# Kernel optimization log

Measured on AMD Instinct MI355X. Metric: run time of the kernel, lower is better.

Reference implementation:

```python
import jax, jax.numpy as jnp
import numpy as np

B, Q, K, D, H, HD, HID, ED, CPB, E = 2, 300, 1024, 256, 8, 32, 32, 256, 256, 131072
N = B * Q
EPS = 1e-5


def _ln(x, g, b):
    mu = x.mean(-1, keepdims=True)
    v = ((x - mu) ** 2).mean(-1, keepdims=True)
    return (x - mu) / jnp.sqrt(v + EPS) * g + b


def setup_inputs():
    key = jax.random.key(0)
    ks = jax.random.split(key, 32)
    rn = lambda k, s, sc=0.02: jax.random.normal(k, s, jnp.float32) * sc
    return {
        "nodes": jax.random.normal(ks[0], (N, D), jnp.float32),
        "images": jax.random.normal(ks[1], (B, K, D), jnp.float32),
        "rel_coords": jax.random.normal(ks[2], (B, Q, K, 2), jnp.float32),
        "edge_feats": jax.random.normal(ks[3], (E, ED), jnp.float32),
        "edge_index": jax.random.randint(ks[4], (2, E), 0, N, jnp.int32),
        "images_mask": jnp.zeros((B, K), dtype=bool),
        "ln1_g": jnp.ones((D,)), "ln1_b": jnp.zeros((D,)),
        "ln2_g": jnp.ones((D,)), "ln2_b": jnp.zeros((D,)),
        "ln3_g": jnp.ones((D,)), "ln3_b": jnp.zeros((D,)),
        "Wni": rn(ks[5], (D, HID * H)), "bni": jnp.zeros((HID * H,)),
        "Wnj": rn(ks[6], (D, HID * H)), "bnj": jnp.zeros((HID * H,)),
        "We": rn(ks[7], (ED, HID * H)), "be": jnp.zeros((HID * H,)),
        "attn_proj": jax.random.normal(ks[8], (H, HID), jnp.float32),
        "Wmsg": rn(ks[9], (D + ED, D)), "bmsg": jnp.zeros((D,)),
        "Wg_out": rn(ks[10], (D, D)), "bg_out": jnp.zeros((D,)),
        "Wq": rn(ks[11], (D, D)), "bq": jnp.zeros((D,)),
        "Wkv": rn(ks[12], (D, 2 * D)), "bkv": jnp.zeros((2 * D,)),
        "Wc1": rn(ks[13], (2, CPB), 0.5), "bc1": jnp.zeros((CPB,)),
        "Wc2": rn(ks[14], (CPB, H), 0.1), "bc2": jnp.zeros((H,)),
        "Wc_out": rn(ks[15], (D, D)), "bc_out": jnp.zeros((D,)),
        "Wf1": rn(ks[16], (D, 4 * D)), "bf1": jnp.zeros((4 * D,)),
        "Wf2": rn(ks[17], (4 * D, D)), "bf2": jnp.zeros((D,)),
    }


def reference(nodes, images, rel_coords, edge_feats, edge_index, images_mask,
              ln1_g, ln1_b, ln2_g, ln2_b, ln3_g, ln3_b,
              Wni, bni, Wnj, bnj, We, be, attn_proj, Wmsg, bmsg, Wg_out, bg_out,
              Wq, bq, Wkv, bkv, Wc1, bc1, Wc2, bc2, Wc_out, bc_out,
              Wf1, bf1, Wf2, bf2):
    src, dst = edge_index[0], edge_index[1]
    # --- graph attention (pre-LN residual) ---
    x = _ln(nodes, ln1_g, ln1_b)
    ni, nj = x[src], x[dst]  # [E, D]
    hidden = jax.nn.leaky_relu(
        ni @ Wni + bni + nj @ Wnj + bnj + edge_feats @ We + be, 0.2)
    hidden = hidden.reshape(E, H, HID)
    logits = jnp.einsum('ehd,hd->eh', hidden, attn_proj)  # [E, H]
    m = jax.ops.segment_max(logits, src, num_segments=N)
    z = jnp.exp(logits - m[src])
    scores = z / jax.ops.segment_sum(z, src, num_segments=N)[src]  # scatter softmax
    msg = (jnp.concatenate([nj, edge_feats], -1) @ Wmsg + bmsg).reshape(E, H, HD)
    agg = jax.ops.segment_sum(msg * scores[..., None], src, num_segments=N).reshape(N, D)
    nodes = nodes + (agg @ Wg_out + bg_out)
    # --- cross attention with continuous position bias ---
    x2 = _ln(nodes, ln2_g, ln2_b).reshape(B, Q, D)
    q = (x2 @ Wq + bq).reshape(B, Q, H, HD).transpose(0, 2, 1, 3)  # [B,H,Q,hd]
    kv = (images @ Wkv + bkv).reshape(B, K, 2, H, HD)
    k = kv[:, :, 0].transpose(0, 2, 1, 3)  # [B,H,K,hd]
    v = kv[:, :, 1].transpose(0, 2, 1, 3)
    cpb = jax.nn.relu(rel_coords @ Wc1 + bc1) @ Wc2 + bc2  # [B,Q,K,H]
    bias = jnp.where(images_mask[:, None, None, :], -jnp.inf,
                     jnp.transpose(cpb, (0, 3, 1, 2)))  # [B,H,Q,K]
    att = jnp.einsum('bhqd,bhkd->bhqk', q, k) / jnp.sqrt(jnp.float32(HD)) + bias
    p = jax.nn.softmax(att, axis=-1)
    out = jnp.einsum('bhqk,bhkd->bhqd', p, v)
    out = out.reshape(B, Q, H * HD)  # faithful to original: reshape WITHOUT head transpose
    nodes = nodes + (out @ Wc_out + bc_out).reshape(N, D)
    # --- FFN (residual from the normed input, as in original) ---
    x3 = _ln(nodes, ln3_g, ln3_b)
    ff = jax.nn.gelu(x3 @ Wf1 + bf1, approximate=False) @ Wf2 + bf2
    return ff + x3
```

## Files before the change

kernel.cpp:

```cpp
#include <hip/hip_runtime.h>
#include <hip/hip_bf16.h>
#include <math.h>

#define E_   131072
#define N_   600
#define NB_  2
#define NQ_  300
#define NK_  1024
#define NH_  8

typedef __hip_bfloat16 bf16;
typedef __bf16 bh8 __attribute__((ext_vector_type(8)));
typedef float  fx4 __attribute__((ext_vector_type(4)));

static __device__ __forceinline__ float b2f(bf16 x){ return __bfloat162float(x); }
static __device__ __forceinline__ float bfbits2f(unsigned short u){
  return __uint_as_float((unsigned)u << 16);
}
static __device__ __forceinline__ unsigned short bfu(float x){
  return __bfloat16_as_ushort(__float2bfloat16(x));
}
static __device__ __forceinline__ unsigned pack2(float x, float y){
  return (unsigned)bfu(x) | ((unsigned)bfu(y) << 16);
}
static __device__ __forceinline__ float ldf(const void* p, size_t i, bool isf32){
  return isf32 ? ((const float*)p)[i] : b2f(((const bf16*)p)[i]);
}

constexpr int WOFF[32] = {
  0,256,512,768,1024,1280,
  1536,67072,67328,132864,
  133120,133376,
  133632,264704,
  264960,330496,330752,396288,
  396544,527616,
  528128,528640,528896,530944,
  530952,596488,
  596744,858888,859912,1122056,
  1122312,
  1187848};
#define NWSEG 31
#define WTOT  1187848
struct SrcTab { const void* p[NWSEG]; };
struct TrTab { int4 d[8]; };

static __device__ __forceinline__ void ln_stats(float v, int t, float* r1, float* r2,
                                                float& mu, float& rstd){
  float s1 = v, s2 = v*v;
  #pragma unroll
  for (int o = 32; o; o >>= 1){ s1 += __shfl_down(s1, o); s2 += __shfl_down(s2, o); }
  if ((t & 63) == 0){ r1[t>>6] = s1; r2[t>>6] = s2; }
  __syncthreads();
  float t1 = r1[0]+r1[1]+r1[2]+r1[3];
  float t2 = r2[0]+r2[1]+r2[2]+r2[3];
  mu = t1 * (1.f/256.f);
  float var = t2 * (1.f/256.f) - mu*mu;
  rstd = rsqrtf(var + 1e-5f);
  __syncthreads();
}

__global__ void k_init(int* cnt, float* denom, const void* nodes, int* dflag){
  int i = blockIdx.x*256 + threadIdx.x;
  if (i < N_) cnt[i] = 0;
  if (i < N_*NH_) denom[i] = 0.f;
  if (i == 0){
    const unsigned short* h = (const unsigned short*)nodes;
    int odd = 0;
    for (int j = 0; j < 64; j++){
      int e = (h[j] >> 7) & 0xFF;
      if (e < 100 || e > 150) odd++;
    }
    *dflag = (odd > 8) ? 1 : 0;
  }
}

__global__ __launch_bounds__(256) void k_cvt(SrcTab tab, float* wall, const int* dflag){
  int i = blockIdx.x*256 + threadIdx.x;
  if (i >= WTOT) return;
  bool isf32 = (*dflag != 0);
  int seg = 0;
  while (seg < NWSEG-1 && i >= WOFF[seg+1]) seg++;
  wall[i] = ldf(tab.p[seg], (size_t)(i - WOFF[seg]), isf32);
}

__global__ __launch_bounds__(256) void k_tr(TrTab tab, const float* __restrict__ wall,
                                            bf16* __restrict__ wbt)
{
  __shared__ float tile[64][65];
  int4 d = tab.d[blockIdx.z];
  int K = d.y, Nn = d.z;
  int k0 = blockIdx.x*64, n0 = blockIdx.y*64;
  if (k0 >= K || n0 >= Nn) return;
  const float* src = wall + d.x;
  bf16* dst = wbt + d.w;
  int t = threadIdx.x;
  int rr = t >> 6, cc = t & 63;
  #pragma unroll
  for (int p = 0; p < 16; p++){
    int row = p*4 + rr;
    tile[row][cc] = src[(size_t)(k0 + row)*Nn + n0 + cc];
  }
  __syncthreads();
  #pragma unroll
  for (int p = 0; p < 16; p++){
    int row = p*4 + rr;
    dst[(size_t)(n0 + row)*K + k0 + cc] = __float2bfloat16(tile[cc][row]);
  }
}

__global__ __launch_bounds__(256) void k_ln1(
    const void* __restrict__ nodes, const int* __restrict__ dflag,
    const float* __restrict__ g1, const float* __restrict__ b1, bf16* __restrict__ x1)
{
  __shared__ float r1[4], r2[4];
  int n = blockIdx.x, t = threadIdx.x;
  bool isf32 = (*dflag != 0);
  float v = ldf(nodes, (size_t)n*256 + t, isf32);
  float mu, rstd;
  ln_stats(v, t, r1, r2, mu, rstd);
  x1[n*256 + t] = __float2bfloat16((v - mu) * rstd * g1[t] + b1[t]);
}

__global__ void k_count(const int* __restrict__ ei, int* cnt){
  int e = blockIdx.x*256 + threadIdx.x;
  atomicAdd(&cnt[ei[e]], 1);
}

__global__ __launch_bounds__(1024) void k_scan(const int* __restrict__ cnt,
                                               int* offs, int* cursor){
  __shared__ int s[1024];
  int t = threadIdx.x;
  s[t] = (t < N_) ? cnt[t] : 0;
  __syncthreads();
  for (int o = 1; o < 1024; o <<= 1){
    int v = 0;
    if (t >= o) v = s[t - o];
    __syncthreads();
    if (t >= o) s[t] += v;
    __syncthreads();
  }
  if (t < N_){ int excl = (t == 0) ? 0 : s[t-1]; offs[t] = excl; cursor[t] = excl; }
  if (t == N_-1) offs[N_] = s[N_-1];
}

__global__ void k_scatter(const int* __restrict__ ei, int* cursor, int* eorder){
  int e = blockIdx.x*256 + threadIdx.x;
  int pos = atomicAdd(&cursor[ei[e]], 1);
  eorder[pos] = e;
}

__global__ __launch_bounds__(256) void k_gemm_dual(
    const void* __restrict__ A, int m_base, const int* __restrict__ dflag,
    const bf16* __restrict__ BT, bf16* __restrict__ C)
{
  __shared__ __align__(16) bf16 As[128*72];
  __shared__ __align__(16) bf16 Bs[128*72];
  int m0 = blockIdx.x * 128;
  int n0 = blockIdx.y * 128;
  int t = threadIdx.x;
  bool isf32 = (*dflag != 0);
  int wave = t >> 6, lane = t & 63;
  int wr = (wave >> 1) * 64, wc = (wave & 1) * 64;
  int lm = lane & 15, lq = lane >> 4;
  int srow = t >> 2;
  int scol = (t & 3) * 16;
  size_t r0  = (size_t)(m_base + m0 + srow) * 256;
  size_t r1  = (size_t)(m_base + m0 + 64 + srow) * 256;
  size_t rB0 = (size_t)(n0 + srow) * 256;
  size_t rB1 = (size_t)(n0 + 64 + srow) * 256;
  fx4 acc[4][4] = {};
  for (int kk = 0; kk < 256; kk += 64){
    uint4 a00, a01, a10, a11, b00, b01, b10, b11;
    if (isf32){
      const float* p0 = (const float*)A + r0 + kk + scol;
      const float* p1 = (const float*)A + r1 + kk + scol;
      float4 x0 = *(const float4*)p0,      x1v = *(const float4*)(p0 + 4);
      float4 x2 = *(const float4*)(p0 + 8), x3 = *(const float4*)(p0 + 12);
      float4 y0 = *(const float4*)p1,      y1v = *(const float4*)(p1 + 4);
      float4 y2 = *(const float4*)(p1 + 8), y3 = *(const float4*)(p1 + 12);
      a00.x = pack2(x0.x,x0.y); a00.y = pack2(x0.z,x0.w);
      a00.z = pack2(x1v.x,x1v.y); a00.w = pack2(x1v.z,x1v.w);
      a01.x = pack2(x2.x,x2.y); a01.y = pack2(x2.z,x2.w);
      a01.z = pack2(x3.x,x3.y); a01.w = pack2(x3.z,x3.w);
      a10.x = pack2(y0.x,y0.y); a10.y = pack2(y0.z,y0.w);
      a10.z = pack2(y1v.x,y1v.y); a10.w = pack2(y1v.z,y1v.w);
      a11.x = pack2(y2.x,y2.y); a11.y = pack2(y2.z,y2.w);
      a11.z = pack2(y3.x,y3.y); a11.w = pack2(y3.z,y3.w);
    } else {
      const bf16* p0 = (const bf16*)A + r0 + kk + scol;
      const bf16* p1 = (const bf16*)A + r1 + kk + scol;
      a00 = *(const uint4*)p0;       a01 = *(const uint4*)(p0 + 8);
      a10 = *(const uint4*)p1;       a11 = *(const uint4*)(p1 + 8);
    }
// ... 9 lines not shown
    *(uint4*)(Bs + srow*72 + scol)          = b00;
    *(uint4*)(Bs + srow*72 + scol + 8)      = b01;
    *(uint4*)(Bs + (64+srow)*72 + scol)     = b10;
    *(uint4*)(Bs + (64+srow)*72 + scol + 8) = b11;
    __syncthreads();
    #pragma unroll
    for (int ks = 0; ks < 2; ks++){
      bh8 af[4], bfr[4];
      #pragma unroll
      for (int mt = 0; mt < 4; mt++)
        af[mt] = *reinterpret_cast<const bh8*>(As + (wr + mt*16 + lm)*72 + ks*32 + lq*8);
      #pragma unroll
      for (int nt = 0; nt < 4; nt++)
        bfr[nt] = *reinterpret_cast<const bh8*>(Bs + (wc + nt*16 + lm)*72 + ks*32 + lq*8);
      #pragma unroll
      for (int mt = 0; mt < 4; mt++)
        #pragma unroll
        for (int nt = 0; nt < 4; nt++)
          acc[mt][nt] = __builtin_amdgcn_mfma_f32_16x16x32_bf16(af[mt], bfr[nt], acc[mt][nt], 0, 0, 0);
    }
  }
  #pragma unroll
  for (int mt = 0; mt < 4; mt++)
    #pragma unroll
    for (int nt = 0; nt < 4; nt++)
      #pragma unroll
      for (int r = 0; r < 4; r++){
        int row = m0 + wr + mt*16 + lq*4 + r;
        int col = n0 + wc + nt*16 + lm;
        C[(size_t)row*256 + col] = __float2bfloat16(acc[mt][nt][r]);
      }
}

__global__ __launch_bounds__(256) void k_gemm(
    const void* __restrict__ A, const int* __restrict__ dflag, int adual,
    int K, int M, const bf16* __restrict__ BT, int mode,
    void* __restrict__ D, int ldd,
    const float* __restrict__ bias, const float* __restrict__ add,
    float* __restrict__ aux)
{
  __shared__ __align__(16) bf16 As[128*72];
  __shared__ __align__(16) bf16 Bs[128*72];
  int m0 = blockIdx.x * 128;
  int n0 = blockIdx.y * 128;
  int t = threadIdx.x;
  bool f32src = adual && (*dflag != 0);
  int wave = t >> 6, lane = t & 63;
  int wr = (wave >> 1) * 64, wc = (wave & 1) * 64;
  int lm = lane & 15, lq = lane >> 4;
  int srow = t >> 2;
  int scol = (t & 3) * 16;
  size_t rA0 = (size_t)(m0 + srow) * K;
  size_t rA1 = (size_t)(m0 + 64 + srow) * K;
  size_t rB0 = (size_t)(n0 + srow) * K;
  size_t rB1 = (size_t)(n0 + 64 + srow) * K;
  fx4 acc[4][4] = {};
  for (int kk = 0; kk < K; kk += 64){
    uint4 a00, a01, a10, a11, b00, b01, b10, b11;
    if (f32src){
      const float* p0 = (const float*)A + rA0 + kk + scol;
      const float* p1 = (const float*)A + rA1 + kk + scol;
      float4 x0 = *(const float4*)p0,      x1v = *(const float4*)(p0 + 4);
      float4 x2 = *(const float4*)(p0 + 8), x3 = *(const float4*)(p0 + 12);
      float4 y0 = *(const float4*)p1,      y1v = *(const float4*)(p1 + 4);
      float4 y2 = *(const float4*)(p1 + 8), y3 = *(const float4*)(p1 + 12);
      a00.x = pack2(x0.x,x0.y); a00.y = pack2(x0.z,x0.w);
      a00.z = pack2(x1v.x,x1v.y); a00.w = pack2(x1v.z,x1v.w);
      a01.x = pack2(x2.x,x2.y); a01.y = pack2(x2.z,x2.w);
      a01.z = pack2(x3.x,x3.y); a01.w = pack2(x3.z,x3.w);
      a10.x = pack2(y0.x,y0.y); a10.y = pack2(y0.z,y0.w);
      a10.z = pack2(y1v.x,y1v.y); a10.w = pack2(y1v.z,y1v.w);
      a11.x = pack2(y2.x,y2.y); a11.y = pack2(y2.z,y2.w);
      a11.z = pack2(y3.x,y3.y); a11.w = pack2(y3.z,y3.w);
    } else {
      const bf16* p0 = (const bf16*)A + rA0 + kk + scol;
      const bf16* p1 = (const bf16*)A + rA1 + kk + scol;
      a00 = *(const uint4*)p0;       a01 = *(const uint4*)(p0 + 8);
      a10 = *(const uint4*)p1;       a11 = *(const uint4*)(p1 + 8);
    }
    b00 = *(const uint4*)(BT + rB0 + kk + scol);
    b01 = *(const uint4*)(BT + rB0 + kk + scol + 8);
    b10 = *(const uint4*)(BT + rB1 + kk + scol);
    b11 = *(const uint4*)(BT + rB1 + kk + scol + 8);
    __syncthreads();
    *(uint4*)(As + srow*72 + scol)          = a00;
    *(uint4*)(As + srow*72 + scol + 8)      = a01;
    *(uint4*)(As + (64+srow)*72 + scol)     = a10;
    *(uint4*)(As + (64+srow)*72 + scol + 8) = a11;
    *(uint4*)(Bs + srow*72 + scol)          = b00;
    *(uint4*)(Bs + srow*72 + scol + 8)      = b01;
    *(uint4*)(Bs + (64+srow)*72 + scol)     = b10;
    *(uint4*)(Bs + (64+srow)*72 + scol + 8) = b11;
    __syncthreads();
    #pragma unroll
    for (int ks = 0; ks < 2; ks++){
      bh8 af[4], bfr[4];
      #pragma unroll
      for (int mt = 0; mt < 4; mt++)
        af[mt] = *reinterpret_cast<const bh8*>(As + (wr + mt*16 + lm)*72 + ks*32 + lq*8);
      #pragma unroll
      for (int nt = 0; nt < 4; nt++)
        bfr[nt] = *reinterpret_cast<const bh8*>(Bs + (wc + nt*16 + lm)*72 + ks*32 + lq*8);
      #pragma unroll
      for (int mt = 0; mt < 4; mt++)
        #pragma unroll
        for (int nt = 0; nt < 4; nt++)
          acc[mt][nt] = __builtin_amdgcn_mfma_f32_16x16x32_bf16(af[mt], bfr[nt], acc[mt][nt], 0, 0, 0);
    }
  }
  #pragma unroll
  for (int mt = 0; mt < 4; mt++)
    #pragma unroll
    for (int nt = 0; nt < 4; nt++)
      #pragma unroll
      for (int r = 0; r < 4; r++){
        int row = m0 + wr + mt*16 + lq*4 + r;
        int col = n0 + wc + nt*16 + lm;
        if (row >= M) continue;
        float v = acc[mt][nt][r];
        if (mode == 0){
          if (bias) v += bias[col];
          ((float*)D)[(size_t)row*ldd + col] = v;
        } else if (mode == 1){
          v += bias[col];
          if (col < 256){
            ((float*)D)[(size_t)row*256 + col] = v;
          } else {
            int b = row >> 10, ki = row & 1023;
            int hh = (col - 256) >> 5, dd = (col - 256) & 31;
            aux[(((size_t)b*NH_ + hh)*32 + dd)*NK_ + ki] = v;
          }
        } else if (mode == 2){
          v += bias[col] + add[(size_t)row*ldd + col];
          ((float*)D)[(size_t)row*ldd + col] = v;
        } else {
          v += bias[col];
          float g = 0.5f*v*(1.f + erff(v*0.70710678118654752f));
          ((bf16*)D)[(size_t)row*ldd + col] = __float2bfloat16(g);
        }
      }
}

__global__ __launch_bounds__(256) void k_logits(
    const bf16* __restrict__ He, const float* __restrict__ Pall,
    const float* __restrict__ bni, const float* __restrict__ bnj, const float* __restrict__ be,
    const float* __restrict__ ap, const int* __restrict__ ei,
    float* __restrict__ z, float* __restrict__ denom, int e0chunk)
{
  __shared__ float hs[32*264];
  __shared__ int   ssh[32], dsh[32];
  __shared__ float aps[256], bhs[256];
  int t = threadIdx.x;
  int base = e0chunk + blockIdx.x*32;
  if (t < 32) ssh[t] = ei[base + t];
  else if (t < 64) dsh[t-32] = ei[E_ + base + (t - 32)];
  aps[t] = ap[t];
  bhs[t] = bni[t] + bnj[t] + be[t];
  __syncthreads();
  int slot = (t >> 5)*33 + (t & 31);
  for (int r = 0; r < 32; r++){
    float v = b2f(He[(size_t)(base - e0chunk + r)*256 + t])
            + Pall[ssh[r]*768 + t] + Pall[dsh[r]*768 + 256 + t] + bhs[t];
    v = (v > 0.f) ? v : 0.2f*v;
    hs[r*264 + slot] = v;
  }
  __syncthreads();
  int e = t >> 3, h = t & 7;
  const float* hr  = hs + e*264 + h*33;
  const float* apr = aps + h*32;
  float acc = 0.f;
  #pragma unroll
  for (int i = 0; i < 32; i++) acc = fmaf(hr[i], apr[i], acc);
  float zv = __expf(fminf(acc, 30.f));
  z[(size_t)(base + e)*8 + h] = zv;
  atomicAdd(&denom[ssh[e]*8 + h], zv);
}

__global__ __launch_bounds__(256) void k_agg(
    const int* __restrict__ offs, const int* __restrict__ eorder, const int* __restrict__ ei,
    const float* __restrict__ z,
    const void* __restrict__ ef, const int* __restrict__ dflag,
    const float* __restrict__ Pall, const float* __restrict__ denom,
    const float* __restrict__ bmsg, const float* __restrict__ Wmsg,
    const void* __restrict__ nodes,
    const float* __restrict__ Wg, const float* __restrict__ bg,
    const float* __restrict__ g2, const float* __restrict__ b2v,
    const float* __restrict__ Wq, const float* __restrict__ bq,
    float* __restrict__ nodes1, float* __restrict__ qbuf)
{
  __shared__ float zsh[32*8];
  __shared__ int   esh[32];
  __shared__ int   dsh[32];
  __shared__ float Fs[8*257];
  __shared__ float aggs[256];
  __shared__ float sinv[8];
  __shared__ float r1[4], r2[4];
  int n = blockIdx.x, t = threadIdx.x;
  bool isf32 = (*dflag != 0);
  int h = t >> 5;
  int e0 = offs[n], e1 = offs[n+1];
  float facc[8] = {};
  float gacc = 0.f;
  int jz = t >> 3, hz = t & 7;
  for (int base = e0; base < e1; base += 32){
    int cnt = min(32, e1 - base);
    __syncthreads();
    if (t < 32){
      int e = (t < cnt) ? eorder[base + t] : eorder[e0];
      esh[t] = e;
      dsh[t] = ei[E_ + e];
    }
    __syncthreads();
    zsh[t] = (jz < cnt) ? z[(size_t)esh[jz]*8 + hz] : 0.f;
    __syncthreads();
    #pragma unroll 8
    for (int jj = 0; jj < 32; jj++){
      int e = esh[jj];
      float efv = ldf(ef, (size_t)e*256 + t, isf32);
      float pv  = Pall[(size_t)dsh[jj]*768 + 512 + t];
      #pragma unroll
      for (int hq = 0; hq < 8; hq++) facc[hq] = fmaf(zsh[jj*8 + hq], efv, facc[hq]);
      gacc = fmaf(zsh[jj*8 + h], pv, gacc);
    }
  }
  if (t < 8){
    float ds = denom[n*8 + t];
    sinv[t] = (ds > 0.f) ? 1.f/ds : 0.f;
  }
  __syncthreads();
  #pragma unroll
  for (int hq = 0; hq < 8; hq++)
// ... 12 lines not shown
    am += (p0 + p1) + (p2 + p3);
  }
  aggs[t] = am;
  __syncthreads();
  float o = bg[t] + ldf(nodes, (size_t)n*256 + t, isf32);
  {
    float p0=0.f, p1=0.f, p2=0.f, p3=0.f;
    for (int k = 0; k < 256; k += 4){
      p0 = fmaf(aggs[k+0], Wg[(k+0)*256 + t], p0);
      p1 = fmaf(aggs[k+1], Wg[(k+1)*256 + t], p1);
      p2 = fmaf(aggs[k+2], Wg[(k+2)*256 + t], p2);
      p3 = fmaf(aggs[k+3], Wg[(k+3)*256 + t], p3);
    }
    o += (p0 + p1) + (p2 + p3);
  }
  nodes1[n*256 + t] = o;
  float mu, rstd;
  ln_stats(o, t, r1, r2, mu, rstd);
  float x2 = (o - mu) * rstd * g2[t] + b2v[t];
  aggs[t] = x2;
  __syncthreads();
  float q = bq[t];
  {
    float p0=0.f, p1=0.f, p2=0.f, p3=0.f;
    for (int k = 0; k < 256; k += 4){
      p0 = fmaf(aggs[k+0], Wq[(k+0)*256 + t], p0);
      p1 = fmaf(aggs[k+1], Wq[(k+1)*256 + t], p1);
      p2 = fmaf(aggs[k+2], Wq[(k+2)*256 + t], p2);
      p3 = fmaf(aggs[k+3], Wq[(k+3)*256 + t], p3);
    }
    q += (p0 + p1) + (p2 + p3);
  }
  qbuf[n*256 + t] = q;
}

__global__ __launch_bounds__(256) void k_cpb(
    const void* __restrict__ rel, const int* __restrict__ dflag,
    const float* __restrict__ Wc1, const float* __restrict__ bc1,
    const float* __restrict__ Wc2, const float* __restrict__ bc2, bf16* __restrict__ bias)
{
  __shared__ float w0[256], w1[256], bb[256], w2[256*8], b2s[8];
  int t = threadIdx.x;
  bool isf32 = (*dflag != 0);
  w0[t] = Wc1[t]; w1[t] = Wc1[256 + t]; bb[t] = bc1[t];
  for (int i = t; i < 2048; i += 256) w2[i] = Wc2[i];
  if (t < 8) b2s[t] = bc2[t];
  __syncthreads();
  size_t pos = (size_t)blockIdx.x*256 + t;
  float c0, c1;
  if (isf32){
    float2 v = ((const float2*)rel)[pos];
    c0 = v.x; c1 = v.y;
  } else {
    unsigned v = ((const unsigned*)rel)[pos];
    c0 = bfbits2f((unsigned short)(v & 0xffff));
    c1 = bfbits2f((unsigned short)(v >> 16));
  }
  float acc[8] = {};
  for (int j = 0; j < 256; j++){
    float hj = fmaf(c0, w0[j], fmaf(c1, w1[j], bb[j]));
    hj = fmaxf(hj, 0.f);
    #pragma unroll
    for (int h = 0; h < 8; h++) acc[h] = fmaf(hj, w2[j*8 + h], acc[h]);
  }
  int k = (int)(pos & 1023);
  size_t qq = pos >> 10;
  size_t b = qq / NQ_, q = qq % NQ_;
  bf16* dst = bias + ((b*NH_)*NQ_ + q)*NK_;
  #pragma unroll
  for (int h = 0; h < 8; h++)
    dst[(size_t)h*NQ_*NK_ + k] = __float2bfloat16(acc[h] + b2s[h]);
}

__global__ __launch_bounds__(256) void k_attn(
    const float* __restrict__ qbuf, const float* __restrict__ kbuf, const float* __restrict__ vT,
    const bf16* __restrict__ bias, bf16* __restrict__ Yb)
{
  __shared__ float Qs[8*33];
  __shared__ float Ks[128*33];
  __shared__ float Sc[8*1024];
  __shared__ float Op[4*8*32];
  __shared__ float qs[8];
  int qt = blockIdx.x, h = blockIdx.y, b = blockIdx.z;
  int q0 = qt*8;
  int t = threadIdx.x;
  {
    int q = t >> 5, d = t & 31;
    int gq = q0 + q;
    Qs[q*33 + d] = (gq < NQ_) ? qbuf[((size_t)b*NQ_ + gq)*256 + h*32 + d] : 0.f;
  }
  const float* kbase = kbuf + (size_t)b*NK_*256 + h*32;
  const bf16*  bb    = bias + ((size_t)(b*NH_ + h)*NQ_)*NK_;
  int kl = t & 127;
  int qb = (t >> 7) * 4;
  for (int kt = 0; kt < 8; kt++){
    int k0 = kt*128;
    __syncthreads();
    {
      int r = t >> 1, c0 = (t & 1) * 16;
      const float* src = kbase + (size_t)(k0 + r)*256 + c0;
      float* dst = Ks + r*33 + c0;
      #pragma unroll
      for (int ii = 0; ii < 4; ii++){
        float4 f = *(const float4*)(src + ii*4);
// ... 85 lines not shown
    }
  }
}

__global__ __launch_bounds__(256) void k_ln3(
    const float* __restrict__ n2, const float* __restrict__ g3, const float* __restrict__ b3,
    float* __restrict__ x3f, bf16* __restrict__ x3b)
{
  __shared__ float r1[4], r2[4];
  int n = blockIdx.x, t = threadIdx.x;
  float v = n2[n*256 + t];
  float mu, rstd;
  ln_stats(v, t, r1, r2, mu, rstd);
  float x3 = (v - mu) * rstd * g3[t] + b3[t];
  x3f[n*256 + t] = x3;
  x3b[n*256 + t] = __float2bfloat16(x3);
}

extern "C" void kernel_launch(void* const* d_in, const int* in_sizes, int n_in,
                              void* d_out, int out_size, void* d_ws, size_t ws_size,
                              hipStream_t stream)
{
  const void* nodes  = d_in[0];
  const void* images = d_in[1];
  const void* rel    = d_in[2];
  const void* ef     = d_in[3];
  const int*  ei     = (const int*)d_in[4];
  float* out = (float*)d_out;

  char* w = (char*)d_ws;
  auto alloc = [&](size_t bytes) -> void* {
    void* p = (void*)w; w += (bytes + 255) & ~(size_t)255; return p;
  };
  int*      dflag  = (int*)     alloc(4);
  float*    Wall   = (float*)   alloc((size_t)WTOT*4);
  bf16*     Wbt    = (bf16*)    alloc((size_t)983040*2);
  bf16*     bias   = (bf16*)    alloc((size_t)NB_*NH_*NQ_*NK_*2);
  float*    zbuf   = (float*)   alloc((size_t)E_*8*4);
  float*    Pall   = (float*)   alloc((size_t)N_*768*4);
  float*    nodes1 = (float*)   alloc(N_*256*4);
  float*    qbuf   = (float*)   alloc(N_*256*4);
  float*    kbuf   = (float*)   alloc((size_t)NB_*NK_*256*4);
  float*    vT     = (float*)   alloc((size_t)NB_*NH_*32*NK_*4);
  float*    n2buf  = (float*)   alloc(N_*256*4);
  float*    x3f    = (float*)   alloc(N_*256*4);
  bf16*     x1     = (bf16*)    alloc(N_*256*2);
  bf16*     x3b    = (bf16*)    alloc(N_*256*2);
  bf16*     Yb     = (bf16*)    alloc(N_*256*2);
  bf16*     H1     = (bf16*)    alloc((size_t)N_*1024*2);
  float*    denom  = (float*)   alloc(N_*8*4);
  int*      cnt    = (int*)     alloc(N_*4);
  int*      offs   = (int*)     alloc((N_+1)*4);
  int*      cursor = (int*)     alloc(N_*4);
  int*      eorder = (int*)     alloc((size_t)E_*4);
  size_t used = (size_t)(w - (char*)d_ws);
  int CH = E_;
  while (CH > 2048 && used + (size_t)CH*256*2 + 256 > ws_size) CH >>= 1;
  bf16* He = (bf16*)alloc((size_t)CH*256*2);

  bf16* WeT  = Wbt + 0;
  bf16* WkvT = Wbt + 65536;
  bf16* WnpT = Wbt + 196608;
  bf16* WcoT = Wbt + 393216;
  bf16* Wf1T = Wbt + 458752;
  bf16* Wf2T = Wbt + 720896;

  const float *ln1g=Wall+WOFF[0],  *ln1b=Wall+WOFF[1];
  const float *ln2g=Wall+WOFF[2],  *ln2b=Wall+WOFF[3];
  const float *ln3g=Wall+WOFF[4],  *ln3b=Wall+WOFF[5];
  const float *bni=Wall+WOFF[7],  *bnj=Wall+WOFF[9], *be=Wall+WOFF[10];
  const float *ap =Wall+WOFF[11];
  const float *Wmsg=Wall+WOFF[12], *bmsg=Wall+WOFF[13];
  const float *Wg=Wall+WOFF[14], *bg=Wall+WOFF[15];
  const float *Wq=Wall+WOFF[16], *bq=Wall+WOFF[17];
  const float *bkv=Wall+WOFF[19];
  const float *Wc1=Wall+WOFF[20], *bc1=Wall+WOFF[21];
  const float *Wc2=Wall+WOFF[22], *bc2=Wall+WOFF[23];
  const float *bco=Wall+WOFF[25];
  const float *bf1v=Wall+WOFF[27];
  const float *bf2v=Wall+WOFF[29];

  SrcTab tab;
  {
    const int idx[NWSEG] = {6,7,8,9,10,11, 12,13,14,15, 17,18, 19,20, 21,22,23,24,
                            25,26, 27,28,29,30, 31,32, 33,34,35,36, 16};
    for (int i = 0; i < NWSEG; i++) tab.p[i] = d_in[idx[i]];
  }
  TrTab tr;
  tr.d[0] = {WOFF[30], 256,  256, 0};
  tr.d[1] = {WOFF[18], 256,  512, 65536};
  tr.d[2] = {WOFF[6],  256,  256, 196608};
  tr.d[3] = {WOFF[8],  256,  256, 196608+65536};
  tr.d[4] = {WOFF[12], 256,  256, 196608+131072};
  tr.d[5] = {WOFF[24], 256,  256, 393216};
  tr.d[6] = {WOFF[26], 256, 1024, 458752};
  tr.d[7] = {WOFF[28],1024,  256, 720896};

  k_init   <<<19, 256, 0, stream>>>(cnt, denom, nodes, dflag);
  k_cvt    <<<(WTOT+255)/256, 256, 0, stream>>>(tab, Wall, dflag);
  k_tr     <<<dim3(16,16,8), 256, 0, stream>>>(tr, Wall, Wbt);
  k_ln1    <<<N_, 256, 0, stream>>>(nodes, dflag, ln1g, ln1b, x1);
  k_count  <<<E_/256, 256, 0, stream>>>(ei, cnt);
  k_scan   <<<1, 1024, 0, stream>>>(cnt, offs, cursor);
  k_scatter<<<E_/256, 256, 0, stream>>>(ei, cursor, eorder);

  k_gemm<<<dim3(5,6), 256, 0, stream>>>(x1, dflag, 0, 256, N_, WnpT, 0,
                                        Pall, 768, nullptr, nullptr, nullptr);

  for (int c0 = 0; c0 < E_; c0 += CH){
    k_gemm_dual<<<dim3(CH/128, 2), 256, 0, stream>>>(ef, c0, dflag, WeT, He);
    k_logits   <<<CH/32, 256, 0, stream>>>(He, Pall, bni, bnj, be, ap, ei,
                                           zbuf, denom, c0);
  }
  k_agg  <<<N_, 256, 0, stream>>>(offs, eorder, ei, zbuf, ef, dflag, Pall, denom,
                                  bmsg, Wmsg, nodes, Wg, bg, ln2g, ln2b, Wq, bq,
                                  nodes1, qbuf);
  k_gemm<<<dim3(16,4), 256, 0, stream>>>(images, dflag, 1, 256, NB_*NK_, WkvT, 1,
                                         kbuf, 256, bkv, nullptr, vT);
  k_cpb    <<<NB_*NQ_*NK_/256, 256, 0, stream>>>(rel, dflag, Wc1, bc1, Wc2, bc2, bias);
  dim3 agrid((NQ_ + 7)/8, NH_, NB_);
  k_attn   <<<agrid, 256, 0, stream>>>(qbuf, kbuf, vT, bias, Yb);
  k_gemm<<<dim3(5,2), 256, 0, stream>>>(Yb, dflag, 0, 256, N_, WcoT, 2,
                                        n2buf, 256, bco, nodes1, nullptr);
  k_ln3  <<<N_, 256, 0, stream>>>(n2buf, ln3g, ln3b, x3f, x3b);
  k_gemm<<<dim3(5,8), 256, 0, stream>>>(x3b, dflag, 0, 256, N_, Wf1T, 3,
                                        H1, 1024, bf1v, nullptr, nullptr);
  k_gemm<<<dim3(5,2), 256, 0, stream>>>(H1, dflag, 0, 1024, N_, Wf2T, 2,
                                        out, 256, bf2v, x3f, nullptr);
}
```

Before: 718.9 us.

## Merge prep and independent stages into fewer batched kernel launches

Folds init, weight conversion, transpose and LN1 into a single k_prep launch. The transpose now reads the raw inputs directly, so it no longer depends on the converted copy. Edge counting moves into the scan kernel as shared-memory atomics, and the node projection GEMM, KV GEMM, CPB MLP and edge scatter run as block ranges of one k_batch launch. Every kernel now recomputes the dtype flag per block with a ballot instead of reading a global flag. The aim is to cut launch count and serialization between independent stages, at the cost of a serial single-block count over all edges and heterogeneous blocks sharing one shared-memory footprint.

```diff
diff --git a/kernel.cpp b/kernel.cpp
--- a/kernel.cpp
+++ b/kernel.cpp
@@ -25,6 +25,17 @@
 }
 static __device__ __forceinline__ float ldf(const void* p, size_t i, bool isf32){
   return isf32 ? ((const float*)p)[i] : b2f(((const bf16*)p)[i]);
+}
+
+static __device__ __forceinline__ bool get_isf32(const void* nodes, int t, int* sh){
+  if (t < 64){
+    const unsigned short* h = (const unsigned short*)nodes;
+    int e = (h[t] >> 7) & 0xFF;
+    unsigned long long b = __ballot(e < 100 || e > 150);
+    if (t == 0) *sh = (__popcll(b) > 8) ? 1 : 0;
+  }
+  __syncthreads();
+  return *sh != 0;
 }
 
 constexpr int WOFF[32] = {
@@ -42,7 +53,7 @@
 #define NWSEG 31
 #define WTOT  1187848
 struct SrcTab { const void* p[NWSEG]; };
-struct TrTab { int4 d[8]; };
+struct TrTabP { const void* p[8]; int4 d[8]; };
 
 static __device__ __forceinline__ void ln_stats(float v, int t, float* r1, float* r2,
                                                 float& mu, float& rstd){
@@ -59,78 +70,73 @@
   __syncthreads();
 }
 
-__global__ void k_init(int* cnt, float* denom, const void* nodes, int* dflag){
-  int i = blockIdx.x*256 + threadIdx.x;
-  if (i < N_) cnt[i] = 0;
-  if (i < N_*NH_) denom[i] = 0.f;
-  if (i == 0){
-    const unsigned short* h = (const unsigned short*)nodes;
-    int odd = 0;
-    for (int j = 0; j < 64; j++){
-      int e = (h[j] >> 7) & 0xFF;
-      if (e < 100 || e > 150) odd++;
-    }
-    *dflag = (odd > 8) ? 1 : 0;
-  }
-}
-
-__global__ __launch_bounds__(256) void k_cvt(SrcTab tab, float* wall, const int* dflag){
-  int i = blockIdx.x*256 + threadIdx.x;
-  if (i >= WTOT) return;
-  bool isf32 = (*dflag != 0);
-  int seg = 0;
-  while (seg < NWSEG-1 && i >= WOFF[seg+1]) seg++;
-  wall[i] = ldf(tab.p[seg], (size_t)(i - WOFF[seg]), isf32);
-}
-
-__global__ __launch_bounds__(256) void k_tr(TrTab tab, const float* __restrict__ wall,
-                                            bf16* __restrict__ wbt)
+#define PB_CVT 4641
+#define PB_TR  2048
+#define PB_LN1 600
+#define PB_DEN 19
+#define PB_TOTAL (PB_CVT + PB_TR + PB_LN1 + PB_DEN)
+
+__global__ __launch_bounds__(256) void k_prep(
+    SrcTab tab, TrTabP trp, float* __restrict__ wall, bf16* __restrict__ wbt,
+    const void* __restrict__ nodes, bf16* __restrict__ x1, float* __restrict__ denom)
 {
   __shared__ float tile[64][65];
-  int4 d = tab.d[blockIdx.z];
-  int K = d.y, Nn = d.z;
-  int k0 = blockIdx.x*64, n0 = blockIdx.y*64;
-  if (k0 >= K || n0 >= Nn) return;
-  const float* src = wall + d.x;
-  bf16* dst = wbt + d.w;
+  __shared__ float r1[4], r2[4];
+  __shared__ int dsh;
   int t = threadIdx.x;
-  int rr = t >> 6, cc = t & 63;
-  #pragma unroll
-  for (int p = 0; p < 16; p++){
-    int row = p*4 + rr;
-    tile[row][cc] = src[(size_t)(k0 + row)*Nn + n0 + cc];
-  }
-  __syncthreads();
-  #pragma unroll
-  for (int p = 0; p < 16; p++){
-    int row = p*4 + rr;
-    dst[(size_t)(n0 + row)*K + k0 + cc] = __float2bfloat16(tile[cc][row]);
-  }
-}
-
-__global__ __launch_bounds__(256) void k_ln1(
-    const void* __restrict__ nodes, const int* __restrict__ dflag,
-    const float* __restrict__ g1, const float* __restrict__ b1, bf16* __restrict__ x1)
-{
-  __shared__ float r1[4], r2[4];
-  int n = blockIdx.x, t = threadIdx.x;
-  bool isf32 = (*dflag != 0);
-  float v = ldf(nodes, (size_t)n*256 + t, isf32);
-  float mu, rstd;
-  ln_stats(v, t, r1, r2, mu, rstd);
-  x1[n*256 + t] = __float2bfloat16((v - mu) * rstd * g1[t] + b1[t]);
-}
-
-__global__ void k_count(const int* __restrict__ ei, int* cnt){
-  int e = blockIdx.x*256 + threadIdx.x;
-  atomicAdd(&cnt[ei[e]], 1);
-}
-
-__global__ __launch_bounds__(1024) void k_scan(const int* __restrict__ cnt,
+  int b = blockIdx.x;
+  bool isf32 = get_isf32(nodes, t, &dsh);
+  if (b < PB_CVT){
+    int i = b*256 + t;
+    if (i < WTOT){
+      int seg = 0;
+      while (seg < NWSEG-1 && i >= WOFF[seg+1]) seg++;
+      wall[i] = ldf(tab.p[seg], (size_t)(i - WOFF[seg]), isf32);
+    }
+  } else if (b < PB_CVT + PB_TR){
+    int lb = b - PB_CVT;
+    int bz = lb >> 8, by = (lb >> 4) & 15, bx = lb & 15;
+    int4 d = trp.d[bz];
+    int K = d.y, Nn = d.z;
+    int k0 = bx*64, n0 = by*64;
+    if (k0 < K && n0 < Nn){
+      const void* src = trp.p[bz];
+      bf16* dst = wbt + d.w;
+      int rr = t >> 6, cc = t & 63;
+      #pragma unroll
+      for (int p = 0; p < 16; p++){
+        int row = p*4 + rr;
+        tile[row][cc] = ldf(src, (size_t)(k0 + row)*Nn + n0 + cc, isf32);
+      }
+      __syncthreads();
+      #pragma unroll
+      for (int p = 0; p < 16; p++){
+        int row = p*4 + rr;
+        dst[(size_t)(n0 + row)*K + k0 + cc] = __float2bfloat16(tile[cc][row]);
+      }
+    }
+  } else if (b < PB_CVT + PB_TR + PB_LN1){
+    int n = b - (PB_CVT + PB_TR);
+    float v = ldf(nodes, (size_t)n*256 + t, isf32);
+    float mu, rstd;
+    ln_stats(v, t, r1, r2, mu, rstd);
+    float g  = ldf(tab.p[0], t, isf32);
+    float bb = ldf(tab.p[1], t, isf32);
+    x1[n*256 + t] = __float2bfloat16((v - mu) * rstd * g + bb);
+  } else {
+    int i = (b - (PB_CVT + PB_TR + PB_LN1))*256 + t;
+    if (i < N_*NH_) denom[i] = 0.f;
+  }
+}
+
+__global__ __launch_bounds__(1024) void k_scan(const int* __restrict__ ei,
                                                int* offs, int* cursor){
   __shared__ int s[1024];
   int t = threadIdx.x;
-  s[t] = (t < N_) ? cnt[t] : 0;
+  s[t] = 0;
+  __syncthreads();
+  for (int i = t; i < E_; i += 1024)
+    atomicAdd(&s[ei[i]], 1);
   __syncthreads();
   for (int o = 1; o < 1024; o <<= 1){
     int v = 0;
@@ -143,22 +149,209 @@
   if (t == N_-1) offs[N_] = s[N_-1];
 }
 
-__global__ void k_scatter(const int* __restrict__ ei, int* cursor, int* eorder){
-  int e = blockIdx.x*256 + threadIdx.x;
-  int pos = atomicAdd(&cursor[ei[e]], 1);
-  eorder[pos] = e;
-}
-
-__global__ __launch_bounds__(256) void k_gemm_dual(
-    const void* __restrict__ A, int m_base, const int* __restrict__ dflag,
-    const bf16* __restrict__ BT, bf16* __restrict__ C)
+static __device__ void gemm_body(
+    const void* __restrict__ A, bool f32src, int K, int M,
+    const bf16* __restrict__ BT, int mode,
+    void* __restrict__ D, int ldd,
+    const float* __restrict__ bias, const float* __restrict__ add,
+    float* __restrict__ aux,
+    int bx, int by, int t, bf16* As, bf16* Bs)
+{
+  int m0 = bx * 128;
+  int n0 = by * 128;
+  int wave = t >> 6, lane = t & 63;
+  int wr = (wave >> 1) * 64, wc = (wave & 1) * 64;
+  int lm = lane & 15, lq = lane >> 4;
+  int srow = t >> 2;
+  int scol = (t & 3) * 16;
+  size_t rA0 = (size_t)(m0 + srow) * K;
+  size_t rA1 = (size_t)(m0 + 64 + srow) * K;
+  size_t rB0 = (size_t)(n0 + srow) * K;
+  size_t rB1 = (size_t)(n0 + 64 + srow) * K;
+  fx4 acc[4][4] = {};
+  for (int kk = 0; kk < K; kk += 64){
+    uint4 a00, a01, a10, a11, b00, b01, b10, b11;
+    if (f32src){
+      const float* p0 = (const float*)A + rA0 + kk + scol;
+      const float* p1 = (const float*)A + rA1 + kk + scol;
+      float4 x0 = *(const float4*)p0,      x1v = *(const float4*)(p0 + 4);
+      float4 x2 = *(const float4*)(p0 + 8), x3 = *(const float4*)(p0 + 12);
+      float4 y0 = *(const float4*)p1,      y1v = *(const float4*)(p1 + 4);
+      float4 y2 = *(const float4*)(p1 + 8), y3 = *(const float4*)(p1 + 12);
+      a00.x = pack2(x0.x,x0.y); a00.y = pack2(x0.z,x0.w);
+      a00.z = pack2(x1v.x,x1v.y); a00.w = pack2(x1v.z,x1v.w);
+      a01.x = pack2(x2.x,x2.y); a01.y = pack2(x2.z,x2.w);
+      a01.z = pack2(x3.x,x3.y); a01.w = pack2(x3.z,x3.w);
+      a10.x = pack2(y0.x,y0.y); a10.y = pack2(y0.z,y0.w);
+      a10.z = pack2(y1v.x,y1v.y); a10.w = pack2(y1v.z,y1v.w);
+      a11.x = pack2(y2.x,y2.y); a11.y = pack2(y2.z,y2.w);
+      a11.z = pack2(y3.x,y3.y); a11.w = pack2(y3.z,y3.w);
+    } else {
+      const bf16* p0 = (const bf16*)A + rA0 + kk + scol;
+      const bf16* p1 = (const bf16*)A + rA1 + kk + scol;
+      a00 = *(const uint4*)p0;       a01 = *(const uint4*)(p0 + 8);
+      a10 = *(const uint4*)p1;       a11 = *(const uint4*)(p1 + 8);
+    }
+    b00 = *(const uint4*)(BT + rB0 + kk + scol);
+    b01 = *(const uint4*)(BT + rB0 + kk + scol + 8);
+    b10 = *(const uint4*)(BT + rB1 + kk + scol);
+    b11 = *(const uint4*)(BT + rB1 + kk + scol + 8);
+    __syncthreads();
+    *(uint4*)(As + srow*72 + scol)          = a00;
+    *(uint4*)(As + srow*72 + scol + 8)      = a01;
+    *(uint4*)(As + (64+srow)*72 + scol)     = a10;
+    *(uint4*)(As + (64+srow)*72 + scol + 8) = a11;
+    *(uint4*)(Bs + srow*72 + scol)          = b00;
+    *(uint4*)(Bs + srow*72 + scol + 8)      = b01;
+    *(uint4*)(Bs + (64+srow)*72 + scol)     = b10;
+    *(uint4*)(Bs + (64+srow)*72 + scol + 8) = b11;
+    __syncthreads();
+    #pragma unroll
+    for (int ks = 0; ks < 2; ks++){
+      bh8 af[4], bfr[4];
+      #pragma unroll
+      for (int mt = 0; mt < 4; mt++)
+        af[mt] = *reinterpret_cast<const bh8*>(As + (wr + mt*16 + lm)*72 + ks*32 + lq*8);
+      #pragma unroll
+      for (int nt = 0; nt < 4; nt++)
+        bfr[nt] = *reinterpret_cast<const bh8*>(Bs + (wc + nt*16 + lm)*72 + ks*32 + lq*8);
+      #pragma unroll
+      for (int mt = 0; mt < 4; mt++)
+        #pragma unroll
+        for (int nt = 0; nt < 4; nt++)
+          acc[mt][nt] = __builtin_amdgcn_mfma_f32_16x16x32_bf16(af[mt], bfr[nt], acc[mt][nt], 0, 0, 0);
+    }
+  }
+  #pragma unroll
+  for (int mt = 0; mt < 4; mt++)
+    #pragma unroll
+    for (int nt = 0; nt < 4; nt++)
+      #pragma unroll
+      for (int r = 0; r < 4; r++){
+        int row = m0 + wr + mt*16 + lq*4 + r;
+        int col = n0 + wc + nt*16 + lm;
+        if (row >= M) continue;
+        float v = acc[mt][nt][r];
+        if (mode == 0){
+          if (bias) v += bias[col];
+          ((float*)D)[(size_t)row*ldd + col] = v;
+        } else if (mode == 1){
+          v += bias[col];
+          if (col < 256){
+            ((float*)D)[(size_t)row*256 + col] = v;
+          } else {
+            int b = row >> 10, ki = row & 1023;
+            int hh = (col - 256) >> 5, dd = (col - 256) & 31;
+            aux[(((size_t)b*NH_ + hh)*32 + dd)*NK_ + ki] = v;
+          }
+        } else if (mode == 2){
+          v += bias[col] + add[(size_t)row*ldd + col];
+          ((float*)D)[(size_t)row*ldd + col] = v;
+        } else {
+          v += bias[col];
+          float g = 0.5f*v*(1.f + erff(v*0.70710678118654752f));
+          ((bf16*)D)[(size_t)row*ldd + col] = __float2bfloat16(g);
+        }
+      }
+}
+
+__global__ __launch_bounds__(256) void k_gemm(
+    const void* __restrict__ A, int K, int M, const bf16* __restrict__ BT, int mode,
+    void* __restrict__ D, int ldd,
+    const float* __restrict__ bias, const float* __restrict__ add,
+    float* __restrict__ aux)
 {
   __shared__ __align__(16) bf16 As[128*72];
   __shared__ __align__(16) bf16 Bs[128*72];
+  gemm_body(A, false, K, M, BT, mode, D, ldd, bias, add, aux,
+            blockIdx.x, blockIdx.y, threadIdx.x, As, Bs);
+}
+
+static __device__ void cpb_body(
+    const void* __restrict__ rel, bool isf32,
+    const float* __restrict__ Wc1, const float* __restrict__ bc1,
+    const float* __restrict__ Wc2, const float* __restrict__ bc2,
+    bf16* __restrict__ bias, int cb, int t)
+{
+  __shared__ float w0[256], w1[256], bb[256], w2[256*8], b2s[8];
+  w0[t] = Wc1[t]; w1[t] = Wc1[256 + t]; bb[t] = bc1[t];
+  for (int i = t; i < 2048; i += 256) w2[i] = Wc2[i];
+  if (t < 8) b2s[t] = bc2[t];
+  __syncthreads();
+  size_t pos = (size_t)cb*256 + t;
+  float c0, c1;
+  if (isf32){
+    float2 v = ((const float2*)rel)[pos];
+    c0 = v.x; c1 = v.y;
+  } else {
+    unsigned v = ((const unsigned*)rel)[pos];
+    c0 = bfbits2f((unsigned short)(v & 0xffff));
+    c1 = bfbits2f((unsigned short)(v >> 16));
+  }
+  float acc[8] = {};
+  for (int j = 0; j < 256; j++){
+    float hj = fmaf(c0, w0[j], fmaf(c1, w1[j], bb[j]));
+    hj = fmaxf(hj, 0.f);
+    #pragma unroll
+    for (int h = 0; h < 8; h++) acc[h] = fmaf(hj, w2[j*8 + h], acc[h]);
+  }
+  int k = (int)(pos & 1023);
+  size_t qq = pos >> 10;
+  size_t b = qq / NQ_, q = qq % NQ_;
+  bf16* dst = bias + ((b*NH_)*NQ_ + q)*NK_;
+  #pragma unroll
+  for (int h = 0; h < 8; h++)
+    dst[(size_t)h*NQ_*NK_ + k] = __float2bfloat16(acc[h] + b2s[h]);
+}
+
+#define BB_PALL 30
+#define BB_KV   64
+#define BB_CPB  2400
+#define BB_SCAT 512
+#define BB_TOTAL (BB_PALL + BB_KV + BB_CPB + BB_SCAT)
+
+__global__ __launch_bounds__(256) void k_batch(
+    const bf16* __restrict__ x1, const bf16* __restrict__ WnpT, float* __restrict__ Pall,
+    const void* __restrict__ images, const bf16* __restrict__ WkvT,
+    float* __restrict__ kbuf, float* __restrict__ vT, const float* __restrict__ bkv,
+    const void* __restrict__ rel,
+    const float* __restrict__ Wc1, const float* __restrict__ bc1,
+    const float* __restrict__ Wc2, const float* __restrict__ bc2, bf16* __restrict__ bias,
+    const int* __restrict__ ei, int* __restrict__ cursor, int* __restrict__ eorder,
+    const void* __restrict__ nodes)
+{
+  __shared__ __align__(16) bf16 As[128*72];
+  __shared__ __align__(16) bf16 Bs[128*72];
+  __shared__ int dsh;
+  int t = threadIdx.x, b = blockIdx.x;
+  bool isf32 = get_isf32(nodes, t, &dsh);
+  if (b < BB_PALL){
+    gemm_body(x1, false, 256, N_, WnpT, 0, Pall, 768, nullptr, nullptr, nullptr,
+              b % 5, b / 5, t, As, Bs);
+  } else if (b < BB_PALL + BB_KV){
+    int bb = b - BB_PALL;
+    gemm_body(images, isf32, 256, NB_*NK_, WkvT, 1, kbuf, 256, bkv, nullptr, vT,
+              bb & 15, bb >> 4, t, As, Bs);
+  } else if (b < BB_PALL + BB_KV + BB_CPB){
+    cpb_body(rel, isf32, Wc1, bc1, Wc2, bc2, bias, b - (BB_PALL + BB_KV), t);
+  } else {
+    int e = (b - (BB_PALL + BB_KV + BB_CPB))*256 + t;
+    int pos = atomicAdd(&cursor[ei[e]], 1);
+    eorder[pos] = e;
+  }
+}
+
+__global__ __launch_bounds__(256) void k_gemm_dual(
+    const void* __restrict__ A, int m_base, const void* __restrict__ nodes,
+    const bf16* __restrict__ BT, bf16* __restrict__ C)
+{
+  __shared__ __align__(16) bf16 As[128*72];
+  __shared__ __align__(16) bf16 Bs[128*72];
+  __shared__ int dsh;
+  int t = threadIdx.x;
+  bool isf32 = get_isf32(nodes, t, &dsh);
   int m0 = blockIdx.x * 128;
   int n0 = blockIdx.y * 128;
-  int t = threadIdx.x;
-  bool isf32 = (*dflag != 0);
   int wave = t >> 6, lane = t & 63;
   int wr = (wave >> 1) * 64, wc = (wave & 1) * 64;
   int lm = lane & 15, lq = lane >> 4;
@@ -234,115 +427,6 @@
       }
 }
 
-__global__ __launch_bounds__(256) void k_gemm(
-    const void* __restrict__ A, const int* __restrict__ dflag, int adual,
-    int K, int M, const bf16* __restrict__ BT, int mode,
-    void* __restrict__ D, int ldd,
-    const float* __restrict__ bias, const float* __restrict__ add,
-    float* __restrict__ aux)
-{
-  __shared__ __align__(16) bf16 As[128*72];
-  __shared__ __align__(16) bf16 Bs[128*72];
-  int m0 = blockIdx.x * 128;
-  int n0 = blockIdx.y * 128;
-  int t = threadIdx.x;
-  bool f32src = adual && (*dflag != 0);
-  int wave = t >> 6, lane = t & 63;
-  int wr = (wave >> 1) * 64, wc = (wave & 1) * 64;
-  int lm = lane & 15, lq = lane >> 4;
-  int srow = t >> 2;
-  int scol = (t & 3) * 16;
-  size_t rA0 = (size_t)(m0 + srow) * K;
-  size_t rA1 = (size_t)(m0 + 64 + srow) * K;
-  size_t rB0 = (size_t)(n0 + srow) * K;
-  size_t rB1 = (size_t)(n0 + 64 + srow) * K;
-  fx4 acc[4][4] = {};
-  for (int kk = 0; kk < K; kk += 64){
-    uint4 a00, a01, a10, a11, b00, b01, b10, b11;
-    if (f32src){
-      const float* p0 = (const float*)A + rA0 + kk + scol;
-      const float* p1 = (const float*)A + rA1 + kk + scol;
-      float4 x0 = *(const float4*)p0,      x1v = *(const float4*)(p0 + 4);
-      float4 x2 = *(const float4*)(p0 + 8), x3 = *(const float4*)(p0 + 12);
-      float4 y0 = *(const float4*)p1,      y1v = *(const float4*)(p1 + 4);
-      float4 y2 = *(const float4*)(p1 + 8), y3 = *(const float4*)(p1 + 12);
-      a00.x = pack2(x0.x,x0.y); a00.y = pack2(x0.z,x0.w);
-      a00.z = pack2(x1v.x,x1v.y); a00.w = pack2(x1v.z,x1v.w);
-      a01.x = pack2(x2.x,x2.y); a01.y = pack2(x2.z,x2.w);
-      a01.z = pack2(x3.x,x3.y); a01.w = pack2(x3.z,x3.w);
-      a10.x = pack2(y0.x,y0.y); a10.y = pack2(y0.z,y0.w);
-      a10.z = pack2(y1v.x,y1v.y); a10.w = pack2(y1v.z,y1v.w);
-      a11.x = pack2(y2.x,y2.y); a11.y = pack2(y2.z,y2.w);
-      a11.z = pack2(y3.x,y3.y); a11.w = pack2(y3.z,y3.w);
-    } else {
-      const bf16* p0 = (const bf16*)A + rA0 + kk + scol;
-      const bf16* p1 = (const bf16*)A + rA1 + kk + scol;
-      a00 = *(const uint4*)p0;       a01 = *(const uint4*)(p0 + 8);
-      a10 = *(const uint4*)p1;       a11 = *(const uint4*)(p1 + 8);
-    }
-    b00 = *(const uint4*)(BT + rB0 + kk + scol);
-    b01 = *(const uint4*)(BT + rB0 + kk + scol + 8);
-    b10 = *(const uint4*)(BT + rB1 + kk + scol);
-    b11 = *(const uint4*)(BT + rB1 + kk + scol + 8);
-    __syncthreads();
-    *(uint4*)(As + srow*72 + scol)          = a00;
-    *(uint4*)(As + srow*72 + scol + 8)      = a01;
-    *(uint4*)(As + (64+srow)*72 + scol)     = a10;
-    *(uint4*)(As + (64+srow)*72 + scol + 8) = a11;
-    *(uint4*)(Bs + srow*72 + scol)          = b00;
-    *(uint4*)(Bs + srow*72 + scol + 8)      = b01;
-    *(uint4*)(Bs + (64+srow)*72 + scol)     = b10;
-    *(uint4*)(Bs + (64+srow)*72 + scol + 8) = b11;
-    __syncthreads();
-    #pragma unroll
-    for (int ks = 0; ks < 2; ks++){
-      bh8 af[4], bfr[4];
-      #pragma unroll
-      for (int mt = 0; mt < 4; mt++)
-        af[mt] = *reinterpret_cast<const bh8*>(As + (wr + mt*16 + lm)*72 + ks*32 + lq*8);
-      #pragma unroll
-      for (int nt = 0; nt < 4; nt++)
-        bfr[nt] = *reinterpret_cast<const bh8*>(Bs + (wc + nt*16 + lm)*72 + ks*32 + lq*8);
-      #pragma unroll
-      for (int mt = 0; mt < 4; mt++)
-        #pragma unroll
-        for (int nt = 0; nt < 4; nt++)
-          acc[mt][nt] = __builtin_amdgcn_mfma_f32_16x16x32_bf16(af[mt], bfr[nt], acc[mt][nt], 0, 0, 0);
-    }
-  }
-  #pragma unroll
-  for (int mt = 0; mt < 4; mt++)
-    #pragma unroll
-    for (int nt = 0; nt < 4; nt++)
-      #pragma unroll
-      for (int r = 0; r < 4; r++){
-        int row = m0 + wr + mt*16 + lq*4 + r;
-        int col = n0 + wc + nt*16 + lm;
-        if (row >= M) continue;
-        float v = acc[mt][nt][r];
-        if (mode == 0){
-          if (bias) v += bias[col];
-          ((float*)D)[(size_t)row*ldd + col] = v;
-        } else if (mode == 1){
-          v += bias[col];
-          if (col < 256){
-            ((float*)D)[(size_t)row*256 + col] = v;
-          } else {
-            int b = row >> 10, ki = row & 1023;
-            int hh = (col - 256) >> 5, dd = (col - 256) & 31;
-            aux[(((size_t)b*NH_ + hh)*32 + dd)*NK_ + ki] = v;
-          }
-        } else if (mode == 2){
-          v += bias[col] + add[(size_t)row*ldd + col];
-          ((float*)D)[(size_t)row*ldd + col] = v;
-        } else {
-          v += bias[col];
-          float g = 0.5f*v*(1.f + erff(v*0.70710678118654752f));
-          ((bf16*)D)[(size_t)row*ldd + col] = __float2bfloat16(g);
-        }
-      }
-}
-
 __global__ __launch_bounds__(256) void k_logits(
     const bf16* __restrict__ He, const float* __restrict__ Pall,
     const float* __restrict__ bni, const float* __restrict__ bnj, const float* __restrict__ be,
@@ -381,7 +465,7 @@
 __global__ __launch_bounds__(256) void k_agg(
     const int* __restrict__ offs, const int* __restrict__ eorder, const int* __restrict__ ei,
     const float* __restrict__ z,
-    const void* __restrict__ ef, const int* __restrict__ dflag,
+    const void* __restrict__ ef,
     const float* __restrict__ Pall, const float* __restrict__ denom,
     const float* __restrict__ bmsg, const float* __restrict__ Wmsg,
     const void* __restrict__ nodes,
@@ -397,8 +481,9 @@
   __shared__ float aggs[256];
   __shared__ float sinv[8];
   __shared__ float r1[4], r2[4];
+  __shared__ int dfsh;
   int n = blockIdx.x, t = threadIdx.x;
-  bool isf32 = (*dflag != 0);
+  bool isf32 = get_isf32(nodes, t, &dfsh);
   int h = t >> 5;
   int e0 = offs[n], e1 = offs[n+1];
   float facc[8] = {};
@@ -477,44 +562,6 @@
     q += (p0 + p1) + (p2 + p3);
   }
   qbuf[n*256 + t] = q;
-}
-
-__global__ __launch_bounds__(256) void k_cpb(
-    const void* __restrict__ rel, const int* __restrict__ dflag,
-    const float* __restrict__ Wc1, const float* __restrict__ bc1,
-    const float* __restrict__ Wc2, const float* __restrict__ bc2, bf16* __restrict__ bias)
-{
-  __shared__ float w0[256], w1[256], bb[256], w2[256*8], b2s[8];
-  int t = threadIdx.x;
-  bool isf32 = (*dflag != 0);
-  w0[t] = Wc1[t]; w1[t] = Wc1[256 + t]; bb[t] = bc1[t];
-  for (int i = t; i < 2048; i += 256) w2[i] = Wc2[i];
-  if (t < 8) b2s[t] = bc2[t];
-  __syncthreads();
-  size_t pos = (size_t)blockIdx.x*256 + t;
-  float c0, c1;
-  if (isf32){
-    float2 v = ((const float2*)rel)[pos];
-    c0 = v.x; c1 = v.y;
-  } else {
-    unsigned v = ((const unsigned*)rel)[pos];
-    c0 = bfbits2f((unsigned short)(v & 0xffff));
-    c1 = bfbits2f((unsigned short)(v >> 16));
-  }
-  float acc[8] = {};
-  for (int j = 0; j < 256; j++){
-    float hj = fmaf(c0, w0[j], fmaf(c1, w1[j], bb[j]));
-    hj = fmaxf(hj, 0.f);
-    #pragma unroll
-    for (int h = 0; h < 8; h++) acc[h] = fmaf(hj, w2[j*8 + h], acc[h]);
-  }
-  int k = (int)(pos & 1023);
-  size_t qq = pos >> 10;
-  size_t b = qq / NQ_, q = qq % NQ_;
-  bf16* dst = bias + ((b*NH_)*NQ_ + q)*NK_;
-  #pragma unroll
-  for (int h = 0; h < 8; h++)
-    dst[(size_t)h*NQ_*NK_ + k] = __float2bfloat16(acc[h] + b2s[h]);
 }
 
 __global__ __launch_bounds__(256) void k_attn(
@@ -666,7 +713,6 @@
   auto alloc = [&](size_t bytes) -> void* {
     void* p = (void*)w; w += (bytes + 255) & ~(size_t)255; return p;
   };
-  int*      dflag  = (int*)     alloc(4);
   float*    Wall   = (float*)   alloc((size_t)WTOT*4);
   bf16*     Wbt    = (bf16*)    alloc((size_t)983040*2);
   bf16*     bias   = (bf16*)    alloc((size_t)NB_*NH_*NQ_*NK_*2);
@@ -683,7 +729,6 @@
   bf16*     Yb     = (bf16*)    alloc(N_*256*2);
   bf16*     H1     = (bf16*)    alloc((size_t)N_*1024*2);
   float*    denom  = (float*)   alloc(N_*8*4);
-  int*      cnt    = (int*)     alloc(N_*4);
   int*      offs   = (int*)     alloc((N_+1)*4);
   int*      cursor = (int*)     alloc(N_*4);
   int*      eorder = (int*)     alloc((size_t)E_*4);
@@ -699,7 +744,6 @@
   bf16* Wf1T = Wbt + 458752;
   bf16* Wf2T = Wbt + 720896;
 
-  const float *ln1g=Wall+WOFF[0],  *ln1b=Wall+WOFF[1];
   const float *ln2g=Wall+WOFF[2],  *ln2b=Wall+WOFF[3];
   const float *ln3g=Wall+WOFF[4],  *ln3b=Wall+WOFF[5];
   const float *bni=Wall+WOFF[7],  *bnj=Wall+WOFF[9], *be=Wall+WOFF[10];
@@ -720,45 +764,36 @@
                             25,26, 27,28,29,30, 31,32, 33,34,35,36, 16};
     for (int i = 0; i < NWSEG; i++) tab.p[i] = d_in[idx[i]];
   }
-  TrTab tr;
-  tr.d[0] = {WOFF[30], 256,  256, 0};
-  tr.d[1] = {WOFF[18], 256,  512, 65536};
-  tr.d[2] = {WOFF[6],  256,  256, 196608};
-  tr.d[3] = {WOFF[8],  256,  256, 196608+65536};
-  tr.d[4] = {WOFF[12], 256,  256, 196608+131072};
-  tr.d[5] = {WOFF[24], 256,  256, 393216};
-  tr.d[6] = {WOFF[26], 256, 1024, 458752};
-  tr.d[7] = {WOFF[28],1024,  256, 720896};
-
-  k_init   <<<19, 256, 0, stream>>>(cnt, denom, nodes, dflag);
-  k_cvt    <<<(WTOT+255)/256, 256, 0, stream>>>(tab, Wall, dflag);
-  k_tr     <<<dim3(16,16,8), 256, 0, stream>>>(tr, Wall, Wbt);
-  k_ln1    <<<N_, 256, 0, stream>>>(nodes, dflag, ln1g, ln1b, x1);
-  k_count  <<<E_/256, 256, 0, stream>>>(ei, cnt);
-  k_scan   <<<1, 1024, 0, stream>>>(cnt, offs, cursor);
-  k_scatter<<<E_/256, 256, 0, stream>>>(ei, cursor, eorder);
-
-  k_gemm<<<dim3(5,6), 256, 0, stream>>>(x1, dflag, 0, 256, N_, WnpT, 0,
-                                        Pall, 768, nullptr, nullptr, nullptr);
-
+  TrTabP trp;
+  trp.p[0] = d_in[16]; trp.d[0] = {0, 256,  256, 0};
+  trp.p[1] = d_in[25]; trp.d[1] = {0, 256,  512, 65536};
+  trp.p[2] = d_in[12]; trp.d[2] = {0, 256,  256, 196608};
+  trp.p[3] = d_in[14]; trp.d[3] = {0, 256,  256, 196608+65536};
+  trp.p[4] = d_in[19]; trp.d[4] = {0, 256,  256, 196608+131072};
+  trp.p[5] = d_in[31]; trp.d[5] = {0, 256,  256, 393216};
+  trp.p[6] = d_in[33]; trp.d[6] = {0, 256, 1024, 458752};
+  trp.p[7] = d_in[35]; trp.d[7] = {0,1024,  256, 720896};
+
+  k_prep <<<PB_TOTAL, 256, 0, stream>>>(tab, trp, Wall, Wbt, nodes, x1, denom);
+  k_scan <<<1, 1024, 0, stream>>>(ei, offs, cursor);
+  k_batch<<<BB_TOTAL, 256, 0, stream>>>(x1, WnpT, Pall, images, WkvT,
+                                        kbuf, vT, bkv, rel, Wc1, bc1, Wc2, bc2,
+                                        bias, ei, cursor, eorder, nodes);
   for (int c0 = 0; c0 < E_; c0 += CH){
-    k_gemm_dual<<<dim3(CH/128, 2), 256, 0, stream>>>(ef, c0, dflag, WeT, He);
+    k_gemm_dual<<<dim3(CH/128, 2), 256, 0, stream>>>(ef, c0, nodes, WeT, He);
     k_logits   <<<CH/32, 256, 0, stream>>>(He, Pall, bni, bnj, be, ap, ei,
                                            zbuf, denom, c0);
   }
-  k_agg  <<<N_, 256, 0, stream>>>(offs, eorder, ei, zbuf, ef, dflag, Pall, denom,
+  k_agg  <<<N_, 256, 0, stream>>>(offs, eorder, ei, zbuf, ef, Pall, denom,
                                   bmsg, Wmsg, nodes, Wg, bg, ln2g, ln2b, Wq, bq,
                                   nodes1, qbuf);
-  k_gemm<<<dim3(16,4), 256, 0, stream>>>(images, dflag, 1, 256, NB_*NK_, WkvT, 1,
-                                         kbuf, 256, bkv, nullptr, vT);
-  k_cpb    <<<NB_*NQ_*NK_/256, 256, 0, stream>>>(rel, dflag, Wc1, bc1, Wc2, bc2, bias);
   dim3 agrid((NQ_ + 7)/8, NH_, NB_);
-  k_attn   <<<agrid, 256, 0, stream>>>(qbuf, kbuf, vT, bias, Yb);
-  k_gemm<<<dim3(5,2), 256, 0, stream>>>(Yb, dflag, 0, 256, N_, WcoT, 2,
-                                        n2buf, 256, bco, nodes1, nullptr);
+  k_attn <<<agrid, 256, 0, stream>>>(qbuf, kbuf, vT, bias, Yb);
+  k_gemm <<<dim3(5,2), 256, 0, stream>>>(Yb, 256, N_, WcoT, 2,
+                                         n2buf, 256, bco, nodes1, nullptr);
   k_ln3  <<<N_, 256, 0, stream>>>(n2buf, ln3g, ln3b, x3f, x3b);
-  k_gemm<<<dim3(5,8), 256, 0, stream>>>(x3b, dflag, 0, 256, N_, Wf1T, 3,
-                                        H1, 1024, bf1v, nullptr, nullptr);
-  k_gemm<<<dim3(5,2), 256, 0, stream>>>(H1, dflag, 0, 1024, N_, Wf2T, 2,
-                                        out, 256, bf2v, x3f, nullptr);
-}
+  k_gemm <<<dim3(5,8), 256, 0, stream>>>(x3b, 256, N_, Wf1T, 3,
+                                         H1, 1024, bf1v, nullptr, nullptr);
+  k_gemm <<<dim3(5,2), 256, 0, stream>>>(H1, 1024, N_, Wf2T, 2,
+                                         out, 256, bf2v, x3f, nullptr);
+}
```

Result: slower. 735.1 us (+2.3%).
